# Performance work log

Hardware: AMD Instinct MI355X
Metric: run time of the kernel (lower is better)

## Reference

```python
import math
import jax, jax.numpy as jnp
import numpy as np

B, T, D_MODEL = 4, 2048, 1024
H, HD = 16, 64            # head_dim = d_model // n_heads
NF = 128                  # n_features
EPS = 1e-6
INV_SQRT_NF = 1.0 / math.sqrt(NF)


def make_orf(key, head_dim, n_features, dtype=jnp.float32):
    """Orthogonal Random Features: QR-orthogonalized gaussian blocks, scaled by sqrt(d)."""
    n_blocks = math.ceil(n_features / head_dim)
    keys = jax.random.split(key, n_blocks)
    blocks = []
    for k in keys:
        g = jax.random.normal(k, (head_dim, head_dim), dtype)
        qm, _ = jnp.linalg.qr(g)
        blocks.append(qm)
    W = jnp.concatenate(blocks, axis=1)[:, :n_features]
    return W * jnp.asarray(math.sqrt(head_dim), dtype)


def setup_inputs() -> dict:
    key = jax.random.key(0)
    k0, k1, k2, k3, k4, k5 = jax.random.split(key, 6)
    s = 1.0 / math.sqrt(D_MODEL)  # torch Linear default init scale
    x = jax.random.normal(k0, (B, T, D_MODEL), jnp.float32)
    Wq = jax.random.uniform(k1, (D_MODEL, H * HD), jnp.float32, -s, s)
    Wk = jax.random.uniform(k2, (D_MODEL, H * HD), jnp.float32, -s, s)
    Wv = jax.random.uniform(k3, (D_MODEL, H * HD), jnp.float32, -s, s)
    Wo = jax.random.uniform(k4, (H * HD, D_MODEL), jnp.float32, -s, s)
    W_feat = make_orf(k5, HD, NF)  # (HD, NF), fresh random buffer (not learned)
    return {"x": x, "Wq": Wq, "Wk": Wk, "Wv": Wv, "Wo": Wo, "W_feat": W_feat}


def _favor_plus(x, W):
    """phi(x) = exp(x.W - ||x||^2/2) / sqrt(NF); x:(B,H,T,HD) -> (B,H,T,NF)."""
    sq = 0.5 * jnp.sum(x * x, axis=-1, keepdims=True)
    return jnp.exp(x @ W - sq) * INV_SQRT_NF


def _causal_linear_attention(qp, kp, v):
    """Causal linear attention scan. qp,kp:(B,H,T,NF), v:(B,H,T,HD) -> (B,H,T,HD)."""
    Bb, Hh = qp.shape[0], qp.shape[1]

    def step(carry, qkv):
        S, z = carry  # S:(B,H,NF,HD), z:(B,H,NF)
        q_t, k_t, v_t = qkv
        S = S + jnp.einsum('bhd,bhe->bhde', k_t, v_t)
        z = z + k_t
        num = jnp.einsum('bhd,bhde->bhe', q_t, S)
        den = jnp.einsum('bhd,bhd->bh', q_t, z) + EPS
        return (S, z), num / den[..., None]

    S0 = jnp.zeros((Bb, Hh, NF, HD), qp.dtype)
    z0 = jnp.zeros((Bb, Hh, NF), qp.dtype)
    xs = (jnp.moveaxis(qp, 2, 0), jnp.moveaxis(kp, 2, 0), jnp.moveaxis(v, 2, 0))
    _, ys = jax.lax.scan(step, (S0, z0), xs)  # ys: (T,B,H,HD)
    return jnp.moveaxis(ys, 0, 2)  # (B,H,T,HD)


def reference(x, Wq, Wk, Wv, Wo, W_feat):
    Bb, Tt, _ = x.shape

    def heads(W):
        return (x @ W).reshape(Bb, Tt, H, HD).transpose(0, 2, 1, 3)  # (B,H,T,HD)

    q, k, v = heads(Wq), heads(Wk), heads(Wv)
    qp = _favor_plus(q, W_feat)
    kp = _favor_plus(k, W_feat)
    y = _causal_linear_attention(qp, kp, v)           # (B,H,T,HD)
    y = y.transpose(0, 2, 1, 3).reshape(Bb, Tt, H * HD)
    return y @ Wo
```

## Files before the change

kernel.cpp:

```cpp
#include <hip/hip_runtime.h>
#include <hip/hip_bf16.h>

typedef unsigned int u32;
typedef unsigned short u16;
typedef __bf16 bf16x8 __attribute__((ext_vector_type(8)));
typedef float f32x4 __attribute__((ext_vector_type(4)));

__device__ __forceinline__ float b2f(u16 s){ union{u32 x; float f;} c; c.x = ((u32)s) << 16; return c.f; }
__device__ __forceinline__ float b2f_lo(u32 u){ union{u32 x; float f;} c; c.x = u << 16; return c.f; }
__device__ __forceinline__ float b2f_hi(u32 u){ union{u32 x; float f;} c; c.x = u & 0xFFFF0000u; return c.f; }
__device__ __forceinline__ u16 f2b(float f){
    union{float f; u32 u;} c; c.f = f;
    u32 r = c.u + 0x7FFFu + ((c.u >> 16) & 1u);
    return (u16)(r >> 16);
}
__device__ __forceinline__ u32 pk(float lo, float hi){
    return (u32)f2b(lo) | ((u32)f2b(hi) << 16);
}
__device__ __forceinline__ void gl_lds16(const u16* g, u16* l){
    __builtin_amdgcn_global_load_lds(
        (const __attribute__((address_space(1))) void*)g,
        (__attribute__((address_space(3))) void*)l, 16, 0, 0);
}


__global__ __launch_bounds__(256) void tobf16(const float* __restrict__ in, u16* __restrict__ out)
{
    size_t i = ((size_t)blockIdx.x * 256 + threadIdx.x) * 8;
    float4 a = *reinterpret_cast<const float4*>(in + i);
    float4 b = *reinterpret_cast<const float4*>(in + i + 4);
    uint4 v; v.x = pk(a.x, a.y); v.y = pk(a.z, a.w); v.z = pk(b.x, b.y); v.w = pk(b.z, b.w);
    *reinterpret_cast<uint4*>(out + i) = v;
}

__global__ __launch_bounds__(256) void transpose_all(const float* __restrict__ Wq, const float* __restrict__ Wk,
                                                     const float* __restrict__ Wv, const float* __restrict__ Wo,
                                                     u16* __restrict__ WTqkv, u16* __restrict__ WTo)
{
    const float* in; u16* out;
    switch (blockIdx.z){
        case 0:  in = Wq; out = WTqkv;           break;
        case 1:  in = Wk; out = WTqkv + 1048576; break;
        case 2:  in = Wv; out = WTqkv + 2097152; break;
        default: in = Wo; out = WTo;             break;
    }
    __shared__ u16 tile[64][72];
    int kb = blockIdx.x * 64, nb = blockIdx.y * 64, tid = threadIdx.x;
#pragma unroll
    for (int i = 0; i < 2; i++){
        int idx = tid + 256*i; int r = idx >> 3; int c8 = (idx & 7) * 8;
        const float* p = &in[(size_t)(kb + r)*1024 + nb + c8];
        float4 lo = *reinterpret_cast<const float4*>(p);
        float4 hi = *reinterpret_cast<const float4*>(p + 4);
        uint4 v;
        v.x = pk(lo.x, lo.y); v.y = pk(lo.z, lo.w);
        v.z = pk(hi.x, hi.y); v.w = pk(hi.z, hi.w);
        *reinterpret_cast<uint4*>(&tile[r][c8]) = v;
    }
    __syncthreads();
#pragma unroll
    for (int i = 0; i < 2; i++){
        int idx = tid + 256*i; int c = idx >> 3; int r8 = (idx & 7) * 8;
        u32 w[4];
#pragma unroll
        for (int j = 0; j < 4; j++)
            w[j] = (u32)tile[r8 + 2*j][c] | ((u32)tile[r8 + 2*j + 1][c] << 16);
        uint4 v; v.x = w[0]; v.y = w[1]; v.z = w[2]; v.w = w[3];
        *reinterpret_cast<uint4*>(&out[(size_t)(nb + c)*1024 + kb + r8]) = v;
    }
}

template<int MODE>
__global__ __launch_bounds__(256) void gemm_async(const u16* __restrict__ A, const u16* __restrict__ BT,
                                                  float* __restrict__ outf, u16* __restrict__ outh)
{
    __shared__ u16 As[128][32];
    __shared__ u16 Bs[128][32];
    int tid = threadIdx.x, lane = tid & 63, w = tid >> 6;
    int m0 = blockIdx.x * 128, n0 = blockIdx.y * 128;
    int wm = (w >> 1) * 64, wn = (w & 1) * 64;
    int fr = lane & 15, fk = (lane >> 4) * 8;
    f32x4 acc[4][4] = {};
    int r0 = 32*w + (lane >> 2), c0 = (lane & 3) * 8;
    const u16* Ag0 = A  + (size_t)(m0 + r0)*1024 + c0;
    const u16* Ag1 = A  + (size_t)(m0 + r0 + 16)*1024 + c0;
    const u16* Bg0 = BT + (size_t)(n0 + r0)*1024 + c0;
    const u16* Bg1 = BT + (size_t)(n0 + r0 + 16)*1024 + c0;
    u16* Al0 = &As[r0][c0];      u16* Al1 = &As[r0 + 16][c0];
    u16* Bl0 = &Bs[r0][c0];      u16* Bl1 = &Bs[r0 + 16][c0];
    for (int k0 = 0; k0 < 1024; k0 += 32){
        __syncthreads();
        gl_lds16(Ag0 + k0, Al0);
        gl_lds16(Ag1 + k0, Al1);
        gl_lds16(Bg0 + k0, Bl0);
        gl_lds16(Bg1 + k0, Bl1);
        __syncthreads();
        bf16x8 af[4], bf[4];
#pragma unroll
        for (int i = 0; i < 4; i++){
            af[i] = *reinterpret_cast<const bf16x8*>(&As[wm + i*16 + fr][fk]);
            bf[i] = *reinterpret_cast<const bf16x8*>(&Bs[wn + i*16 + fr][fk]);
        }
#pragma unroll
        for (int i = 0; i < 4; i++)
#pragma unroll
            for (int j = 0; j < 4; j++)
                acc[i][j] = __builtin_amdgcn_mfma_f32_16x16x32_bf16(af[i], bf[j], acc[i][j], 0, 0, 0);
    }
#pragma unroll
    for (int i = 0; i < 4; i++){
        int row0 = m0 + wm + i*16 + ((lane >> 4) << 2);
#pragma unroll
        for (int j = 0; j < 4; j++){
            int col = n0 + wn + j*16 + fr;
#pragma unroll
            for (int r = 0; r < 4; r++){
                float val = acc[i][j][r];
                int row = row0 + r;
                if (MODE == 2){
                    outf[(size_t)row*1024 + col] = val;
                } else {
                    int which = col >> 10, colw = col & 1023;
                    int h = colw >> 6, d = colw & 63;
                    int bb = row >> 11, t = row & 2047;
                    outh[(size_t)which*8388608 + (((size_t)(bb*16 + h))*2048 + t)*64 + d] = f2b(val);
                }
            }
        }
    }
}

__global__ __launch_bounds__(256) void featmap_mfma(const u16* __restrict__ xh, const float* __restrict__ Wf,
                                                    u16* __restrict__ xp)
{
    __shared__ u16 Xl[128][72];
    __shared__ u16 Wft[128][72];
    __shared__ float sqp[128][8];
    __shared__ float sql[128];
    int tid = threadIdx.x;
    int lane = tid & 63, w = tid >> 6;
    int m = lane & 15, q = lane >> 4;
    const u16* xb = xh + (size_t)blockIdx.x * 128 * 64;
#pragma unroll
    for (int it = 0; it < 4; it++){
        int idx = tid + 256*it;
        int row = idx >> 3, c8 = (idx & 7) * 8;
        uint4 v = *reinterpret_cast<const uint4*>(xb + (size_t)row*64 + c8);
        *reinterpret_cast<uint4*>(&Xl[row][c8]) = v;
        u32 ww[4] = {v.x, v.y, v.z, v.w};
        float s = 0.f;
#pragma unroll
        for (int j = 0; j < 4; j++){
            float a = b2f_lo(ww[j]), bb = b2f_hi(ww[j]);
            s += a*a + bb*bb;
        }
        sqp[row][idx & 7] = s;
    }
#pragma unroll
    for (int it = 0; it < 8; it++){
        int idx = tid + 256*it;
        int d = idx >> 5, f4 = (idx & 31) * 4;
        float4 v = *reinterpret_cast<const float4*>(Wf + d*128 + f4);
        Wft[f4+0][d] = f2b(v.x); Wft[f4+1][d] = f2b(v.y);
        Wft[f4+2][d] = f2b(v.z); Wft[f4+3][d] = f2b(v.w);
    }
    __syncthreads();
    if (tid < 128){
        float s = 0.f;
#pragma unroll
        for (int j = 0; j < 8; j++) s += sqp[tid][j];
        sql[tid] = s;
    }
    f32x4 acc[2][8] = {};
#pragma unroll
    for (int ks = 0; ks < 2; ks++){
        bf16x8 af[2], bf[8];
#pragma unroll
        for (int mt = 0; mt < 2; mt++)
            af[mt] = *reinterpret_cast<const bf16x8*>(&Xl[32*w + mt*16 + m][ks*32 + q*8]);
#pragma unroll
        for (int nt = 0; nt < 8; nt++)
            bf[nt] = *reinterpret_cast<const bf16x8*>(&Wft[nt*16 + m][ks*32 + q*8]);
#pragma unroll
        for (int mt = 0; mt < 2; mt++)
#pragma unroll
            for (int nt = 0; nt < 8; nt++)
                acc[mt][nt] = __builtin_amdgcn_mfma_f32_16x16x32_bf16(af[mt], bf[nt], acc[mt][nt], 0, 0, 0);
    }
    __syncthreads();
    const float c = 0.08838834764831845f;
    u16* xpb = xp + (size_t)blockIdx.x * 128 * 128;
#pragma unroll
    for (int mt = 0; mt < 2; mt++){
#pragma unroll
        for (int r = 0; r < 4; r++){
            int t = 32*w + mt*16 + q*4 + r;
            float hs = 0.5f * sql[t];
#pragma unroll
            for (int nt = 0; nt < 8; nt++){
                int f = nt*16 + m;
                xpb[(size_t)t*128 + f] = f2b(__expf(fminf(acc[mt][nt][r] - hs, 60.f)) * c);
            }
        }
    }
}

struct FM1 { u16 Xl[128][72]; u16 Wft[128][72]; };
union  FMU { FM1 p1; u16 Kpt[128][136]; };
__global__ __launch_bounds__(256) void featmap_sum(const u16* __restrict__ kh, const float* __restrict__ Wf,
                                                   const u16* __restrict__ vh, u16* __restrict__ kp,
                                                   u16* __restrict__ Sa, float* __restrict__ zs)
{
    __shared__ FMU sm;
    __shared__ u16 Vt[64][136];
    __shared__ float sqp[128][8];
    __shared__ float sql[128];
    int blk = blockIdx.x, tid = threadIdx.x;
    int lane = tid & 63, w = tid >> 6;
    int m = lane & 15, q = lane >> 4;
    const u16* xb = kh + (size_t)blk * 128 * 64;
    const u16* vb = vh + (size_t)blk * 128 * 64;
#pragma unroll
    for (int it = 0; it < 4; it++){
        int idx = tid + 256*it;
        int row = idx >> 3, c8 = (idx & 7) * 8;
        uint4 v = *reinterpret_cast<const uint4*>(xb + (size_t)row*64 + c8);
        *reinterpret_cast<uint4*>(&sm.p1.Xl[row][c8]) = v;
        u32 ww[4] = {v.x, v.y, v.z, v.w};
        float s = 0.f;
#pragma unroll
        for (int j = 0; j < 4; j++){
            float a = b2f_lo(ww[j]), bb = b2f_hi(ww[j]);
            s += a*a + bb*bb;
        }
        sqp[row][idx & 7] = s;
    }
#pragma unroll
    for (int it = 0; it < 8; it++){
        int idx = tid + 256*it;
        int d = idx >> 5, f4 = (idx & 31) * 4;
        float4 v = *reinterpret_cast<const float4*>(Wf + d*128 + f4);
        sm.p1.Wft[f4+0][d] = f2b(v.x); sm.p1.Wft[f4+1][d] = f2b(v.y);
        sm.p1.Wft[f4+2][d] = f2b(v.z); sm.p1.Wft[f4+3][d] = f2b(v.w);
    }
#pragma unroll
    for (int it = 0; it < 4; it++){
        int idx = tid + 256*it;
        int t = idx >> 3, d8 = (idx & 7)*8;
        uint4 v = *reinterpret_cast<const uint4*>(vb + (size_t)t*64 + d8);
        u32 ww[4] = {v.x, v.y, v.z, v.w};
#pragma unroll
        for (int j = 0; j < 4; j++){
            Vt[d8 + 2*j][t]     = (u16)(ww[j] & 0xFFFFu);
            Vt[d8 + 2*j + 1][t] = (u16)(ww[j] >> 16);
        }
    }
    __syncthreads();
    if (tid < 128){
        float s = 0.f;
#pragma unroll
        for (int j = 0; j < 8; j++) s += sqp[tid][j];
        sql[tid] = s;
    }
    f32x4 acc[2][8] = {};
#pragma unroll
    for (int ks = 0; ks < 2; ks++){
        bf16x8 af[2], bf[8];
#pragma unroll
        for (int mt = 0; mt < 2; mt++)
            af[mt] = *reinterpret_cast<const bf16x8*>(&sm.p1.Xl[32*w + mt*16 + m][ks*32 + q*8]);
#pragma unroll
        for (int nt = 0; nt < 8; nt++)
            bf[nt] = *reinterpret_cast<const bf16x8*>(&sm.p1.Wft[nt*16 + m][ks*32 + q*8]);
#pragma unroll
        for (int mt = 0; mt < 2; mt++)
#pragma unroll
            for (int nt = 0; nt < 8; nt++)
                acc[mt][nt] = __builtin_amdgcn_mfma_f32_16x16x32_bf16(af[mt], bf[nt], acc[mt][nt], 0, 0, 0);
    }
    __syncthreads();
    const float c = 0.08838834764831845f;
    u16* xpb = kp + (size_t)blk * 128 * 128;
#pragma unroll
    for (int mt = 0; mt < 2; mt++){
#pragma unroll
        for (int r = 0; r < 4; r++){
            int t = 32*w + mt*16 + q*4 + r;
            float hs = 0.5f * sql[t];
#pragma unroll
            for (int nt = 0; nt < 8; nt++){
                int f = nt*16 + m;
                u16 pv = f2b(__expf(fminf(acc[mt][nt][r] - hs, 60.f)) * c);
                xpb[(size_t)t*128 + f] = pv;
                sm.Kpt[f][t] = pv;
            }
        }
    }
    __syncthreads();
    f32x4 acc2[8] = {};
#pragma unroll
    for (int ks = 0; ks < 4; ks++){
        bf16x8 af = *reinterpret_cast<const bf16x8*>(&Vt[16*w + m][ks*32 + q*8]);
        bf16x8 bf[8];
#pragma unroll
        for (int nt = 0; nt < 8; nt++)
            bf[nt] = *reinterpret_cast<const bf16x8*>(&sm.Kpt[nt*16 + m][ks*32 + q*8]);
#pragma unroll
        for (int nt = 0; nt < 8; nt++)
            acc2[nt] = __builtin_amdgcn_mfma_f32_16x16x32_bf16(af, bf[nt], acc2[nt], 0, 0, 0);
    }
    u16* Sb = Sa + (size_t)blk*8192;
#pragma unroll
    for (int nt = 0; nt < 8; nt++){
#pragma unroll
        for (int r = 0; r < 4; r++){
            int d = 16*w + q*4 + r;
            int f = nt*16 + m;
            Sb[(size_t)d*128 + f] = f2b(acc2[nt][r]);
        }
    }
    if (tid < 128){
        float z = 0.f;
#pragma unroll
        for (int t = 0; t < 128; t++) z += b2f(sm.Kpt[tid][t]);
        zs[(size_t)blk*128 + tid] = z;
    }
}

__global__ __launch_bounds__(256) void prefix_chunks(const u16* __restrict__ Sa, u16* __restrict__ Sb,
                                                     float* __restrict__ zs)
{
    int bh = blockIdx.x, seg = blockIdx.y, tid = threadIdx.x;
    const u16* src = Sa + (size_t)bh*16*8192;
    u16*       dst = Sb + (size_t)bh*16*8192;
#pragma unroll
    for (int it = 0; it < 4; it++){
        int e = seg*1024 + it*256 + tid;
        float run = 0.f;
#pragma unroll
        for (int c = 0; c < 16; c++){
            float v = b2f(src[(size_t)c*8192 + e]);
            dst[(size_t)c*8192 + e] = f2b(run);
            run += v;
        }
    }
    if (seg == 0 && tid < 128){
        float run = 0.f; float* zp = zs + (size_t)bh*16*128 + tid;
#pragma unroll
        for (int c = 0; c < 16; c++){ float v = zp[c*128]; zp[c*128] = run; run += v; }
    }
}

__global__ __launch_bounds__(256) void chunk_out(const u16* __restrict__ qp, const u16* __restrict__ kp,
                                                 const u16* __restrict__ vh, const u16* __restrict__ St,
                                                 const float* __restrict__ zs, u16* __restrict__ y2d)
{
    __shared__ u16 P[128][136];
    __shared__ u16 Vt[64][136];
    __shared__ u16 zl[128];
    int blk = blockIdx.x, tid = threadIdx.x;
    int lane = tid & 63, w = tid >> 6;
    int m = lane & 15, q = lane >> 4;
    int bh = blk >> 4, c = blk & 15;
    int b = bh >> 4, h = bh & 15, t0 = c*128;
    const u16* qpb = qp + ((size_t)bh*2048 + t0)*128;
    const u16* kpb = kp + ((size_t)bh*2048 + t0)*128;
    const u16* vb  = vh + ((size_t)bh*2048 + t0)*64;
    const u16* Stb = St + (size_t)blk*8192;

    if (tid < 128) zl[tid] = f2b(zs[(size_t)blk*128 + tid]);
#pragma unroll
    for (int it = 0; it < 4; it++){
        int idx = tid + 256*it;
        int t = idx >> 3, d8 = (idx & 7)*8;
        uint4 v = *reinterpret_cast<const uint4*>(&vb[(size_t)t*64 + d8]);
        u32 ww[4] = {v.x, v.y, v.z, v.w};
#pragma unroll
        for (int j = 0; j < 4; j++){
            Vt[d8 + 2*j][t]     = (u16)(ww[j] & 0xFFFFu);
            Vt[d8 + 2*j + 1][t] = (u16)(ww[j] >> 16);
        }
    }
    {
        int row = tid >> 1, half = tid & 1;
        int i = row >> 4;
        for (int s2 = 16*(i + 1) + half*2; s2 < 128; s2 += 4)
            *reinterpret_cast<u32*>(&P[row][s2]) = 0;
    }
    {
        static const unsigned char TIa[36] = {0,1,1,2,2,2,3,3,3,3,4,4,4,4,4,
                                              5,5,5,5,5,5,6,6,6,6,6,6,6,7,7,7,7,7,7,7,7};
        static const unsigned char TJa[36] = {0,0,1,0,1,2,0,1,2,3,0,1,2,3,4,
                                              0,1,2,3,4,5,0,1,2,3,4,5,6,0,1,2,3,4,5,6,7};
        for (int idx = w; idx < 36; idx += 4){
            int i = TIa[idx], j = TJa[idx];
            f32x4 a = {};
            const u16* arow = qpb + (size_t)(i*16 + m)*128 + q*8;
            const u16* brow = kpb + (size_t)(j*16 + m)*128 + q*8;
#pragma unroll
            for (int ks = 0; ks < 4; ks++){
                bf16x8 af = *reinterpret_cast<const bf16x8*>(arow + ks*32);
                bf16x8 bf = *reinterpret_cast<const bf16x8*>(brow + ks*32);
                a = __builtin_amdgcn_mfma_f32_16x16x32_bf16(af, bf, a, 0, 0, 0);
            }
            int scol = j*16 + m;
#pragma unroll
            for (int r = 0; r < 4; r++){
                int trow = i*16 + q*4 + r;
                P[trow][scol] = (scol <= trow) ? f2b(a[r]) : (u16)0;
            }
        }
    }
    __syncthreads();
    f32x4 acc[2][4] = {};
    f32x4 accd[2] = {};
    bf16x8 ones;
#pragma unroll
    for (int i = 0; i < 8; i++) ones[i] = (__bf16)1.0f;
    for (int ks = 0; ks <= w; ks++){
        bf16x8 af[2], bf4[4];
#pragma unroll
        for (int mt = 0; mt < 2; mt++)
            af[mt] = *reinterpret_cast<const bf16x8*>(&P[32*w + mt*16 + m][ks*32 + q*8]);
#pragma unroll
        for (int nt = 0; nt < 4; nt++)
            bf4[nt] = *reinterpret_cast<const bf16x8*>(&Vt[nt*16 + m][ks*32 + q*8]);
#pragma unroll
        for (int mt = 0; mt < 2; mt++){
#pragma unroll
            for (int nt = 0; nt < 4; nt++)
                acc[mt][nt] = __builtin_amdgcn_mfma_f32_16x16x32_bf16(af[mt], bf4[nt], acc[mt][nt], 0, 0, 0);
            accd[mt] = __builtin_amdgcn_mfma_f32_16x16x32_bf16(af[mt], ones, accd[mt], 0, 0, 0);
        }
    }
#pragma unroll
    for (int ks = 0; ks < 4; ks++){
        bf16x8 af[2], bf4[4];
        bf16x8 zf = *reinterpret_cast<const bf16x8*>(&zl[ks*32 + q*8]);
#pragma unroll
        for (int mt = 0; mt < 2; mt++)
            af[mt] = *reinterpret_cast<const bf16x8*>(qpb + (size_t)(32*w + mt*16 + m)*128 + ks*32 + q*8);
#pragma unroll
        for (int nt = 0; nt < 4; nt++)
            bf4[nt] = *reinterpret_cast<const bf16x8*>(Stb + (size_t)(nt*16 + m)*128 + ks*32 + q*8);
#pragma unroll
        for (int mt = 0; mt < 2; mt++){
#pragma unroll
            for (int nt = 0; nt < 4; nt++)
                acc[mt][nt] = __builtin_amdgcn_mfma_f32_16x16x32_bf16(af[mt], bf4[nt], acc[mt][nt], 0, 0, 0);
            accd[mt] = __builtin_amdgcn_mfma_f32_16x16x32_bf16(af[mt], zf, accd[mt], 0, 0, 0);
        }
    }
#pragma unroll
    for (int mt = 0; mt < 2; mt++){
#pragma unroll
        for (int nt = 0; nt < 4; nt++){
#pragma unroll
            for (int r = 0; r < 4; r++){
                int t = 32*w + mt*16 + q*4 + r;
                int d = nt*16 + m;
                float den = accd[mt][r] + 1e-6f;
                y2d[((size_t)b*2048 + t0 + t)*1024 + h*64 + d] = f2b(acc[mt][nt][r] / den);
            }
        }
    }
}

extern "C" void kernel_launch(void* const* d_in, const int* in_sizes, int n_in,
                              void* d_out, int out_size, void* d_ws, size_t ws_size,
                              hipStream_t stream)
{
    (void)in_sizes; (void)n_in; (void)out_size; (void)ws_size;
    const float* x  = (const float*)d_in[0];
    const float* Wq = (const float*)d_in[1];
    const float* Wk = (const float*)d_in[2];
    const float* Wv = (const float*)d_in[3];
    const float* Wo = (const float*)d_in[4];
    const float* Wf = (const float*)d_in[5];
    float* out = (float*)d_out;
    char* ws = (char*)d_ws;

    u16*   xh    = (u16*)  (ws + 0);
    u16*   Sa    = (u16*)  (ws + 0);
    u16*   qh    = (u16*)  (ws + 16777216);
    u16*   Sbp   = (u16*)  (ws + 16777216);
    u16*   kh    = (u16*)  (ws + 33554432);
    u16*   y2d   = (u16*)  (ws + 33554432);
    u16*   vh    = (u16*)  (ws + 50331648);
    u16*   qp    = (u16*)  (ws + 67108864);
    u16*   kp    = (u16*)  (ws + 100663296);
    u16*   WTqkv = (u16*)  (ws + 134217728);
    u16*   WTo   = (u16*)  (ws + 140509184);
    float* zs    = (float*)(ws + 142606336);

    tobf16<<<4096, 256, 0, stream>>>(x, xh);
    transpose_all<<<dim3(16, 16, 4), 256, 0, stream>>>(Wq, Wk, Wv, Wo, WTqkv, WTo);

    gemm_async<3><<<dim3(64, 24), 256, 0, stream>>>(xh, WTqkv, nullptr, qh);

    featmap_mfma<<<1024, 256, 0, stream>>>(qh, Wf, qp);
    featmap_sum<<<1024, 256, 0, stream>>>(kh, Wf, vh, kp, Sa, zs);

    prefix_chunks<<<dim3(64, 8), 256, 0, stream>>>(Sa, Sbp, zs);
    chunk_out<<<1024, 256, 0, stream>>>(qp, kp, vh, Sbp, zs, y2d);

    gemm_async<2><<<dim3(64, 8), 256, 0, stream>>>(y2d, WTo, out, nullptr);
}
```

Before: 302.1 us.

## Replace GEMM with double-buffered 8-wave 256x128 pipelined kernel with swizzled LDS

Rewrites both projection GEMMs as an 8-wave, 256x128-tile kernel with BK=64. Global-to-LDS async loads are double-buffered and issued in stages that overlap the MFMA phases, and the LDS layout is XOR-swizzled to avoid bank conflicts. Explicit barriers, waitcnt and setprio interleave loads with compute, replacing the old loop that loaded and computed serially with two syncthreads per step. This adds scheduling complexity and larger LDS use (96KB per block), which limits how many blocks fit on a CU.

```diff
diff --git a/kernel.cpp b/kernel.cpp
--- a/kernel.cpp
+++ b/kernel.cpp
@@ -22,6 +22,7 @@
         (const __attribute__((address_space(1))) void*)g,
         (__attribute__((address_space(3))) void*)l, 16, 0, 0);
 }
+#define BARRIER() do { __builtin_amdgcn_s_barrier(); asm volatile("" ::: "memory"); } while(0)
 
 
 __global__ __launch_bounds__(256) void tobf16(const float* __restrict__ in, u16* __restrict__ out)
@@ -71,48 +72,132 @@
 }
 
 template<int MODE>
-__global__ __launch_bounds__(256) void gemm_async(const u16* __restrict__ A, const u16* __restrict__ BT,
+__global__ __launch_bounds__(512, 2) void gemm_8p(const u16* __restrict__ A, const u16* __restrict__ BT,
                                                   float* __restrict__ outf, u16* __restrict__ outh)
 {
-    __shared__ u16 As[128][32];
-    __shared__ u16 Bs[128][32];
-    int tid = threadIdx.x, lane = tid & 63, w = tid >> 6;
-    int m0 = blockIdx.x * 128, n0 = blockIdx.y * 128;
-    int wm = (w >> 1) * 64, wn = (w & 1) * 64;
-    int fr = lane & 15, fk = (lane >> 4) * 8;
+    constexpr int NT = 16;
+    __shared__ u16 lds[2][24576];
+    const int tid = threadIdx.x;
+    const int w = tid >> 6, l = tid & 63;
+    const int wr = w >> 1, wc = w & 1;
+    const int fr = l & 15, q = l >> 4;
+    const int m0 = blockIdx.x * 256, n0 = blockIdx.y * 128;
+
+    const int srow = w*16 + (l >> 3);
+    const int scol = ((l & 7) ^ (srow & 7)) << 3;
+    const u16* Ag = A  + (size_t)(m0 + srow) * 1024 + scol;
+    const u16* Bg = BT + (size_t)(n0 + srow) * 1024 + scol;
+    const int sd = w*1024 + l*8;
+
+    const int colk0 = (q*8)      ^ ((fr & 7) << 3);
+    const int colk1 = (32 + q*8) ^ ((fr & 7) << 3);
+    const int arow = (wr*64 + fr) * 64;
+    const int brow = 16384 + (wc*64 + fr) * 64;
+
     f32x4 acc[4][4] = {};
-    int r0 = 32*w + (lane >> 2), c0 = (lane & 3) * 8;
-    const u16* Ag0 = A  + (size_t)(m0 + r0)*1024 + c0;
-    const u16* Ag1 = A  + (size_t)(m0 + r0 + 16)*1024 + c0;
-    const u16* Bg0 = BT + (size_t)(n0 + r0)*1024 + c0;
-    const u16* Bg1 = BT + (size_t)(n0 + r0 + 16)*1024 + c0;
-    u16* Al0 = &As[r0][c0];      u16* Al1 = &As[r0 + 16][c0];
-    u16* Bl0 = &Bs[r0][c0];      u16* Bl1 = &Bs[r0 + 16][c0];
-    for (int k0 = 0; k0 < 1024; k0 += 32){
-        __syncthreads();
-        gl_lds16(Ag0 + k0, Al0);
-        gl_lds16(Ag1 + k0, Al1);
-        gl_lds16(Bg0 + k0, Bl0);
-        gl_lds16(Bg1 + k0, Bl1);
-        __syncthreads();
-        bf16x8 af[4], bf[4];
-#pragma unroll
-        for (int i = 0; i < 4; i++){
-            af[i] = *reinterpret_cast<const bf16x8*>(&As[wm + i*16 + fr][fk]);
-            bf[i] = *reinterpret_cast<const bf16x8*>(&Bs[wn + i*16 + fr][fk]);
-        }
-#pragma unroll
-        for (int i = 0; i < 4; i++)
-#pragma unroll
-            for (int j = 0; j < 4; j++)
-                acc[i][j] = __builtin_amdgcn_mfma_f32_16x16x32_bf16(af[i], bf[j], acc[i][j], 0, 0, 0);
-    }
+
+#pragma unroll
+    for (int kt = 0; kt < 2; ++kt){
+        u16* Lb = lds[kt];
+#pragma unroll
+        for (int i = 0; i < 2; ++i){
+            gl_lds16(Ag + (size_t)(i*8)*1024       + kt*64, Lb + sd + i*512);
+            gl_lds16(Ag + (size_t)(128 + i*8)*1024 + kt*64, Lb + 8192 + sd + i*512);
+            gl_lds16(Bg + (size_t)(i*8)*1024       + kt*64, Lb + 16384 + sd + i*512);
+        }
+    }
+    asm volatile("s_waitcnt vmcnt(6)" ::: "memory");
+    __builtin_amdgcn_sched_barrier(0);
+    BARRIER();
+
+    for (int t = 0; t < NT; ++t){
+        u16* Lb = lds[t & 1];
+        const int kt = t + 2;
+        const bool st = (kt < NT);
+        bf16x8 af[4][2], bfr[4][2];
+
+#pragma unroll
+        for (int i = 0; i < 4; ++i){
+            af[i][0] = *reinterpret_cast<const bf16x8*>(Lb + arow + i*1024 + colk0);
+            af[i][1] = *reinterpret_cast<const bf16x8*>(Lb + arow + i*1024 + colk1);
+        }
+#pragma unroll
+        for (int j = 0; j < 4; ++j)
+            bfr[j][0] = *reinterpret_cast<const bf16x8*>(Lb + brow + j*1024 + colk0);
+        __builtin_amdgcn_s_barrier();
+        asm volatile("s_waitcnt lgkmcnt(0)" ::: "memory");
+        __builtin_amdgcn_sched_barrier(0);
+        __builtin_amdgcn_s_setprio(1);
+#pragma unroll
+        for (int i = 0; i < 2; ++i)
+#pragma unroll
+            for (int j = 0; j < 4; ++j)
+                acc[i][j] = __builtin_amdgcn_mfma_f32_16x16x32_bf16(af[i][0], bfr[j][0], acc[i][j], 0, 0, 0);
+        __builtin_amdgcn_s_setprio(0);
+        __builtin_amdgcn_sched_barrier(0);
+        BARRIER();
+
+#pragma unroll
+        for (int j = 0; j < 4; ++j)
+            bfr[j][1] = *reinterpret_cast<const bf16x8*>(Lb + brow + j*1024 + colk1);
+        if (st){
+#pragma unroll
+            for (int i = 0; i < 2; ++i){
+                gl_lds16(Ag + (size_t)(i*8)*1024       + kt*64, Lb + sd + i*512);
+                gl_lds16(Ag + (size_t)(128 + i*8)*1024 + kt*64, Lb + 8192 + sd + i*512);
+            }
+        }
+        __builtin_amdgcn_s_barrier();
+        asm volatile("s_waitcnt lgkmcnt(0)" ::: "memory");
+        __builtin_amdgcn_sched_barrier(0);
+        __builtin_amdgcn_s_setprio(1);
+#pragma unroll
+        for (int i = 2; i < 4; ++i)
+#pragma unroll
+            for (int j = 0; j < 4; ++j)
+                acc[i][j] = __builtin_amdgcn_mfma_f32_16x16x32_bf16(af[i][0], bfr[j][0], acc[i][j], 0, 0, 0);
+        __builtin_amdgcn_s_setprio(0);
+        __builtin_amdgcn_sched_barrier(0);
+        BARRIER();
+
+        if (st){
+#pragma unroll
+            for (int i = 0; i < 2; ++i)
+                gl_lds16(Bg + (size_t)(i*8)*1024 + kt*64, Lb + 16384 + sd + i*512);
+        }
+        __builtin_amdgcn_s_barrier();
+        __builtin_amdgcn_s_setprio(1);
+#pragma unroll
+        for (int i = 0; i < 2; ++i)
+#pragma unroll
+            for (int j = 0; j < 4; ++j)
+                acc[i][j] = __builtin_amdgcn_mfma_f32_16x16x32_bf16(af[i][1], bfr[j][1], acc[i][j], 0, 0, 0);
+        __builtin_amdgcn_s_setprio(0);
+        __builtin_amdgcn_sched_barrier(0);
+        BARRIER();
+
+        __builtin_amdgcn_s_setprio(1);
+#pragma unroll
+        for (int i = 2; i < 4; ++i)
+#pragma unroll
+            for (int j = 0; j < 4; ++j)
+                acc[i][j] = __builtin_amdgcn_mfma_f32_16x16x32_bf16(af[i][1], bfr[j][1], acc[i][j], 0, 0, 0);
+        __builtin_amdgcn_s_setprio(0);
+        __builtin_amdgcn_sched_barrier(0);
+        if (t < NT - 2)
+            asm volatile("s_waitcnt vmcnt(6)" ::: "memory");
+        else
+            asm volatile("s_waitcnt vmcnt(0)" ::: "memory");
+        __builtin_amdgcn_sched_barrier(0);
+        BARRIER();
+    }
+
 #pragma unroll
     for (int i = 0; i < 4; i++){
-        int row0 = m0 + wm + i*16 + ((lane >> 4) << 2);
+        int row0 = m0 + wr*64 + i*16 + q*4;
 #pragma unroll
         for (int j = 0; j < 4; j++){
-            int col = n0 + wn + j*16 + fr;
+            int col = n0 + wc*64 + j*16 + fr;
 #pragma unroll
             for (int r = 0; r < 4; r++){
                 float val = acc[i][j][r];
@@ -122,8 +207,8 @@
                 } else {
                     int which = col >> 10, colw = col & 1023;
                     int h = colw >> 6, d = colw & 63;
-                    int bb = row >> 11, t = row & 2047;
-                    outh[(size_t)which*8388608 + (((size_t)(bb*16 + h))*2048 + t)*64 + d] = f2b(val);
+                    int bb = row >> 11, tt = row & 2047;
+                    outh[(size_t)which*8388608 + (((size_t)(bb*16 + h))*2048 + tt)*64 + d] = f2b(val);
                 }
             }
         }
@@ -496,7 +581,7 @@
     tobf16<<<4096, 256, 0, stream>>>(x, xh);
     transpose_all<<<dim3(16, 16, 4), 256, 0, stream>>>(Wq, Wk, Wv, Wo, WTqkv, WTo);
 
-    gemm_async<3><<<dim3(64, 24), 256, 0, stream>>>(xh, WTqkv, nullptr, qh);
+    gemm_8p<3><<<dim3(32, 24), 512, 0, stream>>>(xh, WTqkv, nullptr, qh);
 
     featmap_mfma<<<1024, 256, 0, stream>>>(qh, Wf, qp);
     featmap_sum<<<1024, 256, 0, stream>>>(kh, Wf, vh, kp, Sa, zs);
@@ -504,5 +589,5 @@
     prefix_chunks<<<dim3(64, 8), 256, 0, stream>>>(Sa, Sbp, zs);
     chunk_out<<<1024, 256, 0, stream>>>(qp, kp, vh, Sbp, zs, y2d);
 
-    gemm_async<2><<<dim3(64, 8), 256, 0, stream>>>(y2d, WTo, out, nullptr);
-}
+    gemm_8p<2><<<dim3(32, 8), 512, 0, stream>>>(y2d, WTo, out, nullptr);
+}
```

Measured after the change: 296.3 us. About the same (-1.9%).

## Rewrite GEMM as double-buffered 128x256 tile with swizzled LDS and phased MFMA

Applied to the files above, without the earlier changes.

Replaces the single-buffered 128x128, K=32 GEMM with a 512-thread, 128x256-tile kernel using K=64 steps. Two LDS buffers are staged asynchronously with global_load_lds, so copies for the next tiles overlap MFMA work, and an XOR swizzle is meant to avoid LDS bank conflicts. Waitcnt, sched and priority hints interleave loads with compute. The cost is more LDS per block, hand-managed vmcnt bookkeeping that is fragile, and fewer blocks in the grid.

```diff
diff --git a/kernel.cpp b/kernel.cpp
--- a/kernel.cpp
+++ b/kernel.cpp
@@ -22,6 +22,11 @@
         (const __attribute__((address_space(1))) void*)g,
         (__attribute__((address_space(3))) void*)l, 16, 0, 0);
 }
+#define BARRIER() do { __builtin_amdgcn_s_barrier(); asm volatile("" ::: "memory"); } while(0)
+#define SCB __builtin_amdgcn_sched_barrier(0)
+#define PHASE_GATE() do { asm volatile("" ::: "memory"); __builtin_amdgcn_s_barrier(); \
+    asm volatile("s_waitcnt lgkmcnt(0)" ::: "memory"); SCB; } while(0)
+#define LD8(p) (*reinterpret_cast<const bf16x8*>(p))
 
 
 __global__ __launch_bounds__(256) void tobf16(const float* __restrict__ in, u16* __restrict__ out)
@@ -71,59 +76,123 @@
 }
 
 template<int MODE>
-__global__ __launch_bounds__(256) void gemm_async(const u16* __restrict__ A, const u16* __restrict__ BT,
+__global__ __launch_bounds__(512, 2) void gemm_2p(const u16* __restrict__ A, const u16* __restrict__ BT,
                                                   float* __restrict__ outf, u16* __restrict__ outh)
 {
-    __shared__ u16 As[128][32];
-    __shared__ u16 Bs[128][32];
-    int tid = threadIdx.x, lane = tid & 63, w = tid >> 6;
-    int m0 = blockIdx.x * 128, n0 = blockIdx.y * 128;
-    int wm = (w >> 1) * 64, wn = (w & 1) * 64;
-    int fr = lane & 15, fk = (lane >> 4) * 8;
+    __shared__ u16 lds[2][24576];
+    const int tid = threadIdx.x;
+    const int l = tid & 63, w = tid >> 6;
+    const int wr = w >> 2, wc = w & 3;
+    const int fr = l & 15, q = l >> 4;
+    const int m0 = blockIdx.x * 128, n0 = blockIdx.y * 256;
+
+    const int srow = tid >> 3;
+    const int scol = ((tid & 7) ^ (srow & 7)) << 3;
+    const u16* Ag = A  + (size_t)(m0 + srow) * 1024 + scol;
+    const u16* Bg = BT + (size_t)(n0 + srow) * 1024 + scol;
+    const int sd = tid * 8;
+
+    const int colk0 = (q*8)      ^ ((fr & 7) << 3);
+    const int colk1 = (32 + q*8) ^ ((fr & 7) << 3);
+    const int aoff = (wr*64 + fr) * 64;
+    const int boff = 8192 + (wc*64 + fr) * 64;
+
     f32x4 acc[4][4] = {};
-    int r0 = 32*w + (lane >> 2), c0 = (lane & 3) * 8;
-    const u16* Ag0 = A  + (size_t)(m0 + r0)*1024 + c0;
-    const u16* Ag1 = A  + (size_t)(m0 + r0 + 16)*1024 + c0;
-    const u16* Bg0 = BT + (size_t)(n0 + r0)*1024 + c0;
-    const u16* Bg1 = BT + (size_t)(n0 + r0 + 16)*1024 + c0;
-    u16* Al0 = &As[r0][c0];      u16* Al1 = &As[r0 + 16][c0];
-    u16* Bl0 = &Bs[r0][c0];      u16* Bl1 = &Bs[r0 + 16][c0];
-    for (int k0 = 0; k0 < 1024; k0 += 32){
-        __syncthreads();
-        gl_lds16(Ag0 + k0, Al0);
-        gl_lds16(Ag1 + k0, Al1);
-        gl_lds16(Bg0 + k0, Bl0);
-        gl_lds16(Bg1 + k0, Bl1);
-        __syncthreads();
-        bf16x8 af[4], bf[4];
-#pragma unroll
-        for (int i = 0; i < 4; i++){
-            af[i] = *reinterpret_cast<const bf16x8*>(&As[wm + i*16 + fr][fk]);
-            bf[i] = *reinterpret_cast<const bf16x8*>(&Bs[wn + i*16 + fr][fk]);
-        }
-#pragma unroll
-        for (int i = 0; i < 4; i++)
-#pragma unroll
-            for (int j = 0; j < 4; j++)
-                acc[i][j] = __builtin_amdgcn_mfma_f32_16x16x32_bf16(af[i], bf[j], acc[i][j], 0, 0, 0);
-    }
-#pragma unroll
-    for (int i = 0; i < 4; i++){
-        int row0 = m0 + wm + i*16 + ((lane >> 4) << 2);
-#pragma unroll
-        for (int j = 0; j < 4; j++){
-            int col = n0 + wn + j*16 + fr;
-#pragma unroll
-            for (int r = 0; r < 4; r++){
-                float val = acc[i][j][r];
+    bf16x8 af[4][2], bf[2][2];
+
+    auto stgA = [&](int buf, int kt){
+#pragma unroll
+        for (int i = 0; i < 2; ++i)
+            gl_lds16(Ag + (size_t)(i*64)*1024 + kt*64, &lds[buf][i*4096 + sd]);
+    };
+    auto stgB = [&](int buf, int kt){
+#pragma unroll
+        for (int j = 0; j < 4; ++j)
+            gl_lds16(Bg + (size_t)(j*64)*1024 + kt*64, &lds[buf][8192 + j*4096 + sd]);
+    };
+
+    stgA(0, 0); stgB(0, 0); stgA(1, 1);
+    asm volatile("s_waitcnt vmcnt(2)" ::: "memory");
+    SCB;
+    BARRIER();
+
+#pragma unroll 1
+    for (int uu = 0; uu < 8; ++uu){
+        const bool s = (uu < 7);
+
+#pragma unroll
+        for (int par = 0; par < 2; ++par){
+            u16* Lb = &lds[par][0];
+            const int ktB = 2*uu + 1 + par;
+            const int ktA = 2*uu + 2 + par;
+            const bool sB = (par == 0) ? true : s;
+            const bool sA = s;
+
+#pragma unroll
+            for (int mt = 0; mt < 4; ++mt){
+                af[mt][0] = LD8(Lb + aoff + mt*1024 + colk0);
+                af[mt][1] = LD8(Lb + aoff + mt*1024 + colk1);
+            }
+#pragma unroll
+            for (int nt = 0; nt < 2; ++nt){
+                bf[nt][0] = LD8(Lb + boff + nt*1024 + colk0);
+                bf[nt][1] = LD8(Lb + boff + nt*1024 + colk1);
+            }
+            if (sB) stgB(par ^ 1, ktB);
+            PHASE_GATE();
+            __builtin_amdgcn_s_setprio(1);
+#pragma unroll
+            for (int mt = 0; mt < 4; ++mt)
+#pragma unroll
+                for (int nt = 0; nt < 2; ++nt){
+                    acc[mt][nt] = __builtin_amdgcn_mfma_f32_16x16x32_bf16(af[mt][0], bf[nt][0], acc[mt][nt], 0, 0, 0);
+                    acc[mt][nt] = __builtin_amdgcn_mfma_f32_16x16x32_bf16(af[mt][1], bf[nt][1], acc[mt][nt], 0, 0, 0);
+                }
+            __builtin_amdgcn_s_setprio(0);
+            SCB;
+            BARRIER();
+
+#pragma unroll
+            for (int nt = 0; nt < 2; ++nt){
+                bf[nt][0] = LD8(Lb + boff + (2+nt)*1024 + colk0);
+                bf[nt][1] = LD8(Lb + boff + (2+nt)*1024 + colk1);
+            }
+            if (sA) stgA(par, ktA);
+            PHASE_GATE();
+            __builtin_amdgcn_s_setprio(1);
+#pragma unroll
+            for (int mt = 0; mt < 4; ++mt)
+#pragma unroll
+                for (int nt = 0; nt < 2; ++nt){
+                    acc[mt][2+nt] = __builtin_amdgcn_mfma_f32_16x16x32_bf16(af[mt][0], bf[nt][0], acc[mt][2+nt], 0, 0, 0);
+                    acc[mt][2+nt] = __builtin_amdgcn_mfma_f32_16x16x32_bf16(af[mt][1], bf[nt][1], acc[mt][2+nt], 0, 0, 0);
+                }
+            __builtin_amdgcn_s_setprio(0);
+            SCB;
+            if (sA) asm volatile("s_waitcnt vmcnt(2)" ::: "memory");
+            else    asm volatile("s_waitcnt vmcnt(0)" ::: "memory");
+            SCB;
+            BARRIER();
+        }
+    }
+
+#pragma unroll
+    for (int mt = 0; mt < 4; ++mt){
+        int row0 = m0 + wr*64 + mt*16 + q*4;
+#pragma unroll
+        for (int nt = 0; nt < 4; ++nt){
+            int col = n0 + wc*64 + nt*16 + fr;
+#pragma unroll
+            for (int r = 0; r < 4; ++r){
+                float val = acc[mt][nt][r];
                 int row = row0 + r;
                 if (MODE == 2){
                     outf[(size_t)row*1024 + col] = val;
                 } else {
                     int which = col >> 10, colw = col & 1023;
                     int h = colw >> 6, d = colw & 63;
-                    int bb = row >> 11, t = row & 2047;
-                    outh[(size_t)which*8388608 + (((size_t)(bb*16 + h))*2048 + t)*64 + d] = f2b(val);
+                    int bb = row >> 11, tt = row & 2047;
+                    outh[(size_t)which*8388608 + (((size_t)(bb*16 + h))*2048 + tt)*64 + d] = f2b(val);
                 }
             }
         }
@@ -496,7 +565,7 @@
     tobf16<<<4096, 256, 0, stream>>>(x, xh);
     transpose_all<<<dim3(16, 16, 4), 256, 0, stream>>>(Wq, Wk, Wv, Wo, WTqkv, WTo);
 
-    gemm_async<3><<<dim3(64, 24), 256, 0, stream>>>(xh, WTqkv, nullptr, qh);
+    gemm_2p<3><<<dim3(64, 12), 512, 0, stream>>>(xh, WTqkv, nullptr, qh);
 
     featmap_mfma<<<1024, 256, 0, stream>>>(qh, Wf, qp);
     featmap_sum<<<1024, 256, 0, stream>>>(kh, Wf, vh, kp, Sa, zs);
@@ -504,5 +573,5 @@
     prefix_chunks<<<dim3(64, 8), 256, 0, stream>>>(Sa, Sbp, zs);
     chunk_out<<<1024, 256, 0, stream>>>(qp, kp, vh, Sbp, zs, y2d);
 
-    gemm_async<2><<<dim3(64, 8), 256, 0, stream>>>(y2d, WTo, out, nullptr);
-}
+    gemm_2p<2><<<dim3(64, 4), 512, 0, stream>>>(y2d, WTo, out, nullptr);
+}
```

Measured after the change: 292.9 us. 1.03x faster.
